# Kernel optimization log

Measured on AMD Instinct MI355X. Metric: run time of the kernel, lower is better.

Reference implementation:

```python
import jax, jax.numpy as jnp
import numpy as np

N_ODE_STEPS = 8  # fixed-step dopri5 in place of adaptive dopri5 (rtol=atol=1e-3)

# Dormand-Prince 5(4) tableau (5th-order solution weights); f is autonomous so c is unused
_A = [
    [1/5],
    [3/40, 9/40],
    [44/45, -56/15, 32/9],
    [19372/6561, -25360/2187, 64448/6561, -212/729],
    [9017/3168, -355/33, 46732/5247, 49/176, -5103/18656],
]
_B = [35/384, 0.0, 500/1113, 125/192, -2187/6784, 11/84]


def setup_inputs() -> dict:
    key = jax.random.key(0)
    ks = jax.random.split(key, 20)
    T, D, H = 128, 1024, 2048
    s = lambda fan: 1.0 / np.sqrt(fan)
    inp = {
        "visit_x": jax.random.normal(ks[0], (T, D), jnp.float32),
        "delta_t": jax.random.uniform(ks[1], (T,), jnp.float32) * 0.1,
        "proj_in_w": jax.random.normal(ks[2], (H, D), jnp.float32) * s(D),
        "proj_in_b": jax.random.normal(ks[3], (H,), jnp.float32) * s(D),
        "ode_w1": jax.random.normal(ks[4], (H, H), jnp.float32) * s(H),
        "ode_b1": jax.random.normal(ks[5], (H,), jnp.float32) * s(H),
        "ode_w2": jax.random.normal(ks[6], (H, H), jnp.float32) * s(H),
        "ode_b2": jax.random.normal(ks[7], (H,), jnp.float32) * s(H),
        "gru_wih": jax.random.normal(ks[8], (3 * H, D), jnp.float32) * s(H),
        "gru_whh": jax.random.normal(ks[9], (3 * H, H), jnp.float32) * s(H),
        "gru_bih": jax.random.normal(ks[10], (3 * H,), jnp.float32) * s(H),
        "gru_bhh": jax.random.normal(ks[11], (3 * H,), jnp.float32) * s(H),
        "proj_out_w": jax.random.normal(ks[12], (D, H), jnp.float32) * s(H),
        "proj_out_b": jax.random.normal(ks[13], (D,), jnp.float32) * s(H),
        "att_w1": jax.random.normal(ks[14], (H, H), jnp.float32) * s(H),
        "att_b1": jax.random.normal(ks[15], (H,), jnp.float32) * s(H),
        "att_w2": jax.random.normal(ks[16], (H,), jnp.float32) * s(H),
        "att_b2": jax.random.normal(ks[17], (1,), jnp.float32) * s(H),
    }
    return inp


def reference(visit_x, delta_t, proj_in_w, proj_in_b, ode_w1, ode_b1, ode_w2,
              ode_b2, gru_wih, gru_whh, gru_bih, gru_bhh, proj_out_w,
              proj_out_b, att_w1, att_b1, att_w2, att_b2):
    H = proj_in_w.shape[0]

    def odef(h):  # [H] -> [H]
        return jnp.tanh(h @ ode_w1.T + ode_b1) @ ode_w2.T + ode_b2

    def dopri5_step(h, dt):
        k = [odef(h)]
        for row in _A:
            acc = h + dt * sum(a * ki for a, ki in zip(row, k))
            k.append(odef(acc))
        return h + dt * sum(b * ki for b, ki in zip(_B, k))

    def ode_interval(h, dt_total):
        dt = dt_total / N_ODE_STEPS
        def body(hc, _):
            return dopri5_step(hc, dt), None
        h_out, _ = jax.lax.scan(body, h, None, length=N_ODE_STEPS)
        return h_out

    def gru(x, h):  # torch GRUCell math, gate order r,z,n
        gi = x @ gru_wih.T + gru_bih
        gh = h @ gru_whh.T + gru_bhh
        gi_r, gi_z, gi_n = jnp.split(gi, 3)
        gh_r, gh_z, gh_n = jnp.split(gh, 3)
        r = jax.nn.sigmoid(gi_r + gh_r)
        z = jax.nn.sigmoid(gi_z + gh_z)
        n = jnp.tanh(gi_n + r * gh_n)
        return (1.0 - z) * n + z * h

    h0 = visit_x[0] @ proj_in_w.T + proj_in_b  # [H]

    def visit_step(h, xs):
        x_i, dt_i = xs
        h_ode = ode_interval(h, dt_i)
        h_new = gru(x_i, h_ode)
        return h_new, h_new

    # interval lengths t_i - t_{i-1} == delta_t[i] (cumsum diff)
    _, hs = jax.lax.scan(visit_step, h0, (visit_x[1:], delta_t[1:]))
    Hmat = jnp.concatenate([h0[None, :], hs], axis=0)  # [T, H]

    scores = jnp.tanh(Hmat @ att_w1.T + att_b1) @ att_w2 + att_b2[0]  # [T]
    alpha = jax.nn.softmax(scores, axis=0)
    visit_x_new = Hmat @ proj_out_w.T + proj_out_b  # [T, D]
    return (visit_x_new, alpha)
```

## Files before the change

### kernel.cpp

```cpp
#include <hip/hip_runtime.h>

typedef unsigned int u32;

#define T    128
#define D    1024
#define HH   2048
#define NWG  256
#define NTH  256
#define NGRP 16
#define GSZ  16

#define WS_SCORES 3072
#define WS_Y      4096
#define WS_HX     8192

constexpr float DP_A[5][5] = {
  {1.f/5.f, 0.f, 0.f, 0.f, 0.f},
  {3.f/40.f, 9.f/40.f, 0.f, 0.f, 0.f},
  {44.f/45.f, -56.f/15.f, 32.f/9.f, 0.f, 0.f},
  {19372.f/6561.f, -25360.f/2187.f, 64448.f/6561.f, -212.f/729.f, 0.f},
  {9017.f/3168.f, -355.f/33.f, 46732.f/5247.f, 49.f/176.f, -5103.f/18656.f}};
#define B0 (35.f/384.f)
#define B2 (500.f/1113.f)
#define B3 (125.f/192.f)
#define B4 (-2187.f/6784.f)
#define B5 (11.f/84.f)

__device__ inline void ld4(const float* p, float* f){
  float4 q = *reinterpret_cast<const float4*>(p);
  f[0]=q.x; f[1]=q.y; f[2]=q.z; f[3]=q.w;
}
__device__ inline void ld8(const float* p, float* f){
  float4 q0 = *reinterpret_cast<const float4*>(p);
  float4 q1 = *reinterpret_cast<const float4*>(p+4);
  f[0]=q0.x; f[1]=q0.y; f[2]=q0.z; f[3]=q0.w;
  f[4]=q1.x; f[5]=q1.y; f[6]=q1.z; f[7]=q1.w;
}
__device__ inline float dot8r(const float* w, const float* v){
  float s = w[0]*v[0];
  s += w[1]*v[1]; s += w[2]*v[2]; s += w[3]*v[3];
  s += w[4]*v[4]; s += w[5]*v[5]; s += w[6]*v[6]; s += w[7]*v[7];
  return s;
}
__device__ inline void cst(float* p, float v){
  __hip_atomic_store(p, v, __ATOMIC_RELAXED, __HIP_MEMORY_SCOPE_AGENT);
}
__device__ inline float cld(const float* p){
  return __hip_atomic_load(p, __ATOMIC_RELAXED, __HIP_MEMORY_SCOPE_AGENT);
}
__device__ inline void cld8(const float* p, float* f){
#pragma unroll
  for (int e=0;e<8;++e) f[e]=cld(p+e);
}

template<int NR>
__device__ inline void wave_reduce(float* p){
#pragma unroll
  for (int r=0;r<NR;++r){
    float v=p[r];
#pragma unroll
    for (int m=1;m<64;m<<=1) v += __shfl_xor(v, m, 64);
    p[r]=v;
  }
}

__device__ inline void garrive(int* bar, int ep, int tid, int g){
  __syncthreads();
  if (tid==0){
    int old = __hip_atomic_fetch_add(bar + 64*(g>>4), 1,
                                     __ATOMIC_RELAXED, __HIP_MEMORY_SCOPE_AGENT);
    if (old == ep*GSZ - 1){
      int rold = __hip_atomic_fetch_add(bar + 1024, 1,
                                        __ATOMIC_RELAXED, __HIP_MEMORY_SCOPE_AGENT);
      if (rold == ep*NGRP - 1){
#pragma unroll
        for (int i=0;i<NGRP;++i)
          __hip_atomic_store(bar + 1088 + 64*i, ep,
                             __ATOMIC_RELAXED, __HIP_MEMORY_SCOPE_AGENT);
      }
    }
  }
}
__device__ inline void gwait(int* bar, int ep, int& dead, int tid, int g){
  int bad=0;
  if (tid==0){
    int guard=0;
    while (__hip_atomic_load(bar + 1088 + 64*(g>>4),
                             __ATOMIC_RELAXED, __HIP_MEMORY_SCOPE_AGENT) < ep){
      __builtin_amdgcn_s_sleep(4);
      if (++guard > (1<<18)) { bad=1; break; }
    }
  }
  if (__syncthreads_count(bad)) dead=1;
}
__device__ inline void gbar(int* bar, int& ep, int& dead, int tid, int g){
  ++ep;
  if (dead) return;
  garrive(bar, ep, tid, g);
  gwait(bar, ep, dead, tid, g);
}

__global__ __launch_bounds__(NTH, 1) void vode_kernel(
  const float* __restrict__ vx,  const float* __restrict__ dts,
  const float* __restrict__ piw, const float* __restrict__ pib,
  const float* __restrict__ w1,  const float* __restrict__ b1,
  const float* __restrict__ w2,  const float* __restrict__ b2,
  const float* __restrict__ wih, const float* __restrict__ whh,
  const float* __restrict__ bih, const float* __restrict__ bhh,
  const float* __restrict__ pow_,const float* __restrict__ pob,
  const float* __restrict__ aw1, const float* __restrict__ ab1,
  const float* __restrict__ aw2,
  float* __restrict__ out, float* __restrict__ ws)
{
  const int g = blockIdx.x, tid = threadIdx.x;
  const int wv = tid>>6, ln = tid&63;
  int*   bar    = (int*)ws;
  float* scores = ws + WS_SCORES;
  float* ybuf   = ws + WS_Y;
  float* hx     = ws + WS_HX;
  int ep = 0, dead = 0;

  __shared__ float part[4][24];
  __shared__ float zb[8], c8[8], b18[8], b28[8];
  __shared__ float myj[6][8], krow[6][8], hrow[8];
  __shared__ float gi_lds[24], gh_lds[24], red8[8];

  float Mr[8][8];
#pragma unroll
  for (int r=0;r<8;++r)
#pragma unroll
    for (int e=0;e<8;++e) Mr[r][e]=0.f;
  for (int m=0;m<HH;++m){
    float w2s[8]; ld8(w2 + (size_t)m*HH + 8*tid, w2s);
#pragma unroll
    for (int r=0;r<8;++r){
      float w1v = w1[(size_t)(8*g+r)*HH + m];
#pragma unroll
      for (int e=0;e<8;++e) Mr[r][e] += w1v*w2s[e];
    }
  }
  {
    float b2s[8]; ld8(b2 + 8*tid, b2s);
    float p[8];
#pragma unroll
    for (int r=0;r<8;++r){
      float w1s[8]; ld8(w1 + (size_t)(8*g+r)*HH + 8*tid, w1s);
      p[r]=dot8r(w1s,b2s);
    }
    wave_reduce<8>(p);
    if (ln==0){
#pragma unroll
      for (int r=0;r<8;++r) part[wv][r]=p[r];
    }
    __syncthreads();
    if (tid<8){
      c8[tid]=part[0][tid]+part[1][tid]+part[2][tid]+part[3][tid];
      b18[tid]=b1[8*g+tid]; b28[tid]=b2[8*g+tid];
    }
    __syncthreads();
  }
  float w2r[8][8];
#pragma unroll
  for (int r=0;r<8;++r) ld8(w2 + (size_t)(8*g+r)*HH + 8*tid, w2r[r]);

  float hsl[8];

  auto zb_compute = [&](){
    float p[8];
#pragma unroll
    for (int r=0;r<8;++r){
      float wr[8]; ld8(w1 + (size_t)(8*g+r)*HH + 8*tid, wr);
      p[r]=dot8r(wr,hsl);
    }
    wave_reduce<8>(p);
    if (ln==0){
#pragma unroll
      for (int r=0;r<8;++r) part[wv][r]=p[r];
    }
    __syncthreads();
    if (tid<8) zb[tid]=part[0][tid]+part[1][tid]+part[2][tid]+part[3][tid];
    __syncthreads();
  };

  auto att_proj = [&](int t){
    float p[12];
#pragma unroll
    for (int r=0;r<8;++r){
      float wr[8]; ld8(aw1 + (size_t)(8*g+r)*HH + 8*tid, wr);
      p[r]=dot8r(wr,hsl);
    }
#pragma unroll
    for (int r=0;r<4;++r){
      float wr[8]; ld8(pow_ + (size_t)(4*g+r)*HH + 8*tid, wr);
      p[8+r]=dot8r(wr,hsl);
    }
    wave_reduce<12>(p);
    if (ln==0){
#pragma unroll
      for (int r=0;r<12;++r) part[wv][r]=p[r];
    }
    __syncthreads();
    if (tid<8){
      float u = tanhf(part[0][tid]+part[1][tid]+part[2][tid]+part[3][tid]
                      + ab1[8*g+tid]);
      red8[tid] = u * aw2[8*g+tid];
    } else if (tid<12){
      int d = 4*g + (tid-8);
      out[(size_t)t*D + d] =
        part[0][tid]+part[1][tid]+part[2][tid]+part[3][tid] + pob[d];
    }
    __syncthreads();
    if (tid==0){
      float s = red8[0]+red8[1]+red8[2]+red8[3]+red8[4]+red8[5]+red8[6]+red8[7];
      atomicAdd(&scores[t], s);
    }
    __syncthreads();
  };

  {
    float x0[4]; ld4(vx + 4*tid, x0);
    float p[8];
#pragma unroll
    for (int r=0;r<8;++r){
      float wr[4]; ld4(piw + (size_t)(8*g+r)*D + 4*tid, wr);
      p[r] = wr[0]*x0[0]+wr[1]*x0[1]+wr[2]*x0[2]+wr[3]*x0[3];
    }
    wave_reduce<8>(p);
    if (ln==0){
#pragma unroll
      for (int r=0;r<8;++r) part[wv][r]=p[r];
    }
    __syncthreads();
    if (tid<8)
      cst(&hx[8*g+tid],
          part[0][tid]+part[1][tid]+part[2][tid]+part[3][tid] + pib[8*g+tid]);
    gbar(bar, ep, dead, tid, g);
    cld8(hx + 8*tid, hsl);
    if (tid<8) hrow[tid] = cld(&hx[8*g+tid]);
    __syncthreads();
    zb_compute();
  }

  int pp = 0;
  int pend = 0;
  for (int t=1; t<T; ++t){
    float dt = dts[t] * 0.125f;

    {
      float xt[4]; ld4(vx + (size_t)t*D + 4*tid, xt);
      float p[24];
#pragma unroll
      for (int rr=0;rr<24;++rr){
        size_t row = (size_t)(rr>>3)*HH + 8*g + (rr&7);
        float wr[4]; ld4(wih + row*D + 4*tid, wr);
        p[rr] = wr[0]*xt[0]+wr[1]*xt[1]+wr[2]*xt[2]+wr[3]*xt[3];
      }
      wave_reduce<24>(p);
      if (ln==0){
#pragma unroll
        for (int rr=0;rr<24;++rr) part[wv][rr]=p[rr];
      }
      __syncthreads();
      if (tid<24){
        size_t row = (size_t)(tid>>3)*HH + 8*g + (tid&7);
        gi_lds[tid] = part[0][tid]+part[1][tid]+part[2][tid]+part[3][tid]
                      + bih[row];
      }
      __syncthreads();
    }

    for (int st=0; st<8; ++st){
#pragma unroll
      for (int s=0;s<6;++s){
        if (tid<8){
          float z = zb[tid];
          if (s>0){
            float sm = 0.f;
#pragma unroll
            for (int j=0;j<5;++j)
              if (j < s) sm += DP_A[s-1][j]*(myj[j][tid]+c8[tid]);
            z += dt*sm;
          }
          cst(&ybuf[pp*HH + 8*g+tid], tanhf(z + b18[tid]));
        }
        ++ep;
        if (!dead) garrive(bar, ep, tid, g);
        if (st==0 && s==0) att_proj(pend);
        if (!dead) gwait(bar, ep, dead, tid, g);
        float ysl[8]; cld8(ybuf + pp*HH + 8*tid, ysl);
        pp ^= 1;
        float p[16];
#pragma unroll
        for (int r=0;r<8;++r){
          p[r]   = dot8r(Mr[r],  ysl);
          p[8+r] = dot8r(w2r[r], ysl);
        }
        wave_reduce<16>(p);
        if (ln==0){
#pragma unroll
          for (int r=0;r<16;++r) part[wv][r]=p[r];
        }
        __syncthreads();
        if (tid<8)
          myj[s][tid] = part[0][tid]+part[1][tid]+part[2][tid]+part[3][tid];
        else if (tid<16)
          krow[s][tid-8] = part[0][tid]+part[1][tid]+part[2][tid]+part[3][tid]
                           + b28[tid-8];
        __syncthreads();
      }
      if (tid<8){
        hrow[tid] += dt*( B0*krow[0][tid] + B2*krow[2][tid] + B3*krow[3][tid]
                        + B4*krow[4][tid] + B5*krow[5][tid] );
        zb[tid]   += dt*( B0*(myj[0][tid]+c8[tid]) + B2*(myj[2][tid]+c8[tid])
                        + B3*(myj[3][tid]+c8[tid]) + B4*(myj[4][tid]+c8[tid])
                        + B5*(myj[5][tid]+c8[tid]) );
      }
      __syncthreads();
    }

    if (tid<8) cst(&hx[8*g+tid], hrow[tid]);
    gbar(bar, ep, dead, tid, g);
    cld8(hx + 8*tid, hsl);
    {
      float p[24];
#pragma unroll
      for (int rr=0;rr<24;++rr){
        size_t row = (size_t)(rr>>3)*HH + 8*g + (rr&7);
        float wr[8]; ld8(whh + row*HH + 8*tid, wr);
        p[rr]=dot8r(wr, hsl);
      }
      wave_reduce<24>(p);
      if (ln==0){
#pragma unroll
        for (int rr=0;rr<24;++rr) part[wv][rr]=p[rr];
      }
      __syncthreads();
      if (tid<24){
        size_t row=(size_t)(tid>>3)*HH + 8*g + (tid&7);
        gh_lds[tid]=part[0][tid]+part[1][tid]+part[2][tid]+part[3][tid]+bhh[row];
      }
      __syncthreads();
      if (tid<8){
        float r_ = 1.f/(1.f+__expf(-(gi_lds[tid]   + gh_lds[tid])));
        float z_ = 1.f/(1.f+__expf(-(gi_lds[8+tid] + gh_lds[8+tid])));
        float n_ = tanhf(gi_lds[16+tid] + r_*gh_lds[16+tid]);
        float hn = (1.f-z_)*n_ + z_*hrow[tid];
        hrow[tid] = hn;
        cst(&hx[HH + 8*g+tid], hn);
      }
      gbar(bar, ep, dead, tid, g);
      cld8(hx + HH + 8*tid, hsl);
      zb_compute();
      pend = t;
    }
  }

  att_proj(T-1);
  gbar(bar, ep, dead, tid, g);

  if (g==0 && tid==0){
    float sc[T];
    for (int i=0;i<T;++i) sc[i]=cld(&scores[i]);
    float mx=-1e30f;
    for (int i=0;i<T;++i) if (sc[i]>mx) mx=sc[i];
    float sum=0.f;
    for (int i=0;i<T;++i) sum += __expf(sc[i]-mx);
    for (int i=0;i<T;++i)
      out[(size_t)T*D + i] = __expf(sc[i]-mx)/sum;
  }
}

extern "C" void kernel_launch(void* const* d_in, const int* in_sizes, int n_in,
                              void* d_out, int out_size, void* d_ws, size_t ws_size,
                              hipStream_t stream){
  hipMemsetAsync(d_ws, 0, 16384, stream);
  vode_kernel<<<dim3(NWG), dim3(NTH), 0, stream>>>(
      (const float*)d_in[0],  (const float*)d_in[1],  (const float*)d_in[2],
      (const float*)d_in[3],  (const float*)d_in[4],  (const float*)d_in[5],
      (const float*)d_in[6],  (const float*)d_in[7],  (const float*)d_in[8],
      (const float*)d_in[9],  (const float*)d_in[10], (const float*)d_in[11],
      (const float*)d_in[12], (const float*)d_in[13], (const float*)d_in[14],
      (const float*)d_in[15], (const float*)d_in[16],
      (float*)d_out, (float*)d_ws);
}
```

Before: 29.43 ms.

## Flatten grid barrier to 64 counters polled by a wave, overlap GRU input projection

Replaces the two-level hierarchical grid barrier (group counters plus root counter plus release flags) with 64 padded counters, each incremented by four workgroups. Every workgroup's first wave polls all 64 counters in parallel with a shorter sleep, which removes the serial release chain on each of the many per-step barriers. The GRU input projection x_t·W_ih is moved out of the serial path into the gap between arrive and wait of the second ODE stage barrier, hiding its weight loads behind barrier latency. The cost is more polling traffic on the atomic counters from 256 waves and a larger workspace memset.

```diff
diff --git a/kernel.cpp b/kernel.cpp
--- a/kernel.cpp
+++ b/kernel.cpp
@@ -7,12 +7,10 @@
 #define HH   2048
 #define NWG  256
 #define NTH  256
-#define NGRP 16
-#define GSZ  16
-
-#define WS_SCORES 3072
-#define WS_Y      4096
-#define WS_HX     8192
+
+#define WS_SCORES 4096
+#define WS_Y      6144
+#define WS_HX     10240
 
 constexpr float DP_A[5][5] = {
   {1.f/5.f, 0.f, 0.f, 0.f, 0.f},
@@ -64,30 +62,19 @@
   }
 }
 
-__device__ inline void garrive(int* bar, int ep, int tid, int g){
+__device__ inline void garrive(int* bar, int tid, int g){
   __syncthreads();
-  if (tid==0){
-    int old = __hip_atomic_fetch_add(bar + 64*(g>>4), 1,
-                                     __ATOMIC_RELAXED, __HIP_MEMORY_SCOPE_AGENT);
-    if (old == ep*GSZ - 1){
-      int rold = __hip_atomic_fetch_add(bar + 1024, 1,
-                                        __ATOMIC_RELAXED, __HIP_MEMORY_SCOPE_AGENT);
-      if (rold == ep*NGRP - 1){
-#pragma unroll
-        for (int i=0;i<NGRP;++i)
-          __hip_atomic_store(bar + 1088 + 64*i, ep,
-                             __ATOMIC_RELAXED, __HIP_MEMORY_SCOPE_AGENT);
-      }
-    }
-  }
-}
-__device__ inline void gwait(int* bar, int ep, int& dead, int tid, int g){
+  if (tid==0)
+    __hip_atomic_fetch_add(bar + 64*(g>>2), 1,
+                           __ATOMIC_RELAXED, __HIP_MEMORY_SCOPE_AGENT);
+}
+__device__ inline void gwait(int* bar, int ep, int& dead, int tid){
   int bad=0;
-  if (tid==0){
+  if (tid<64){
     int guard=0;
-    while (__hip_atomic_load(bar + 1088 + 64*(g>>4),
-                             __ATOMIC_RELAXED, __HIP_MEMORY_SCOPE_AGENT) < ep){
-      __builtin_amdgcn_s_sleep(4);
+    while (__hip_atomic_load(bar + 64*tid,
+                             __ATOMIC_RELAXED, __HIP_MEMORY_SCOPE_AGENT) < 4*ep){
+      __builtin_amdgcn_s_sleep(1);
       if (++guard > (1<<18)) { bad=1; break; }
     }
   }
@@ -96,8 +83,8 @@
 __device__ inline void gbar(int* bar, int& ep, int& dead, int tid, int g){
   ++ep;
   if (dead) return;
-  garrive(bar, ep, tid, g);
-  gwait(bar, ep, dead, tid, g);
+  garrive(bar, tid, g);
+  gwait(bar, ep, dead, tid);
 }
 
 __global__ __launch_bounds__(NTH, 1) void vode_kernel(
@@ -217,6 +204,29 @@
     __syncthreads();
   };
 
+  auto gi_compute = [&](int t){
+    float xt[4]; ld4(vx + (size_t)t*D + 4*tid, xt);
+    float p[24];
+#pragma unroll
+    for (int rr=0;rr<24;++rr){
+      size_t row = (size_t)(rr>>3)*HH + 8*g + (rr&7);
+      float wr[4]; ld4(wih + row*D + 4*tid, wr);
+      p[rr] = wr[0]*xt[0]+wr[1]*xt[1]+wr[2]*xt[2]+wr[3]*xt[3];
+    }
+    wave_reduce<24>(p);
+    if (ln==0){
+#pragma unroll
+      for (int rr=0;rr<24;++rr) part[wv][rr]=p[rr];
+    }
+    __syncthreads();
+    if (tid<24){
+      size_t row = (size_t)(tid>>3)*HH + 8*g + (tid&7);
+      gi_lds[tid] = part[0][tid]+part[1][tid]+part[2][tid]+part[3][tid]
+                    + bih[row];
+    }
+    __syncthreads();
+  };
+
   {
     float x0[4]; ld4(vx + 4*tid, x0);
     float p[8];
@@ -245,29 +255,6 @@
   int pend = 0;
   for (int t=1; t<T; ++t){
     float dt = dts[t] * 0.125f;
-
-    {
-      float xt[4]; ld4(vx + (size_t)t*D + 4*tid, xt);
-      float p[24];
-#pragma unroll
-      for (int rr=0;rr<24;++rr){
-        size_t row = (size_t)(rr>>3)*HH + 8*g + (rr&7);
-        float wr[4]; ld4(wih + row*D + 4*tid, wr);
-        p[rr] = wr[0]*xt[0]+wr[1]*xt[1]+wr[2]*xt[2]+wr[3]*xt[3];
-      }
-      wave_reduce<24>(p);
-      if (ln==0){
-#pragma unroll
-        for (int rr=0;rr<24;++rr) part[wv][rr]=p[rr];
-      }
-      __syncthreads();
-      if (tid<24){
-        size_t row = (size_t)(tid>>3)*HH + 8*g + (tid&7);
-        gi_lds[tid] = part[0][tid]+part[1][tid]+part[2][tid]+part[3][tid]
-                      + bih[row];
-      }
-      __syncthreads();
-    }
 
     for (int st=0; st<8; ++st){
 #pragma unroll
@@ -284,9 +271,12 @@
           cst(&ybuf[pp*HH + 8*g+tid], tanhf(z + b18[tid]));
         }
         ++ep;
-        if (!dead) garrive(bar, ep, tid, g);
-        if (st==0 && s==0) att_proj(pend);
-        if (!dead) gwait(bar, ep, dead, tid, g);
+        if (!dead) garrive(bar, tid, g);
+        if (st==0){
+          if (s==0) att_proj(pend);
+          else if (s==1) gi_compute(t);
+        }
+        if (!dead) gwait(bar, ep, dead, tid);
         float ysl[8]; cld8(ybuf + pp*HH + 8*tid, ysl);
         pp ^= 1;
         float p[16];
@@ -373,7 +363,7 @@
 extern "C" void kernel_launch(void* const* d_in, const int* in_sizes, int n_in,
                               void* d_out, int out_size, void* d_ws, size_t ws_size,
                               hipStream_t stream){
-  hipMemsetAsync(d_ws, 0, 16384, stream);
+  hipMemsetAsync(d_ws, 0, 20480, stream);
   vode_kernel<<<dim3(NWG), dim3(NTH), 0, stream>>>(
       (const float*)d_in[0],  (const float*)d_in[1],  (const float*)d_in[2],
       (const float*)d_in[3],  (const float*)d_in[4],  (const float*)d_in[5],
```

New measurement: 31.59 ms (median of 3 runs). 1.07x slower.
